# Kernel tuning notes

Hardware: AMD Instinct MI355X
Metric: run time of the kernel (lower is better)

Reference implementation:

```python
import jax, jax.numpy as jnp
import numpy as np

N = 384
C_Z = 128
N_HEADS = 4
HEAD_DIM = C_Z // N_HEADS
LN_EPS = 1e-5


def _layernorm(x, w, b):
    mu = jnp.mean(x, axis=-1, keepdims=True)
    var = jnp.mean(jnp.square(x - mu), axis=-1, keepdims=True)
    return (x - mu) * jax.lax.rsqrt(var + LN_EPS) * w + b


def setup_inputs() -> dict:
    key = jax.random.key(0)
    ks = jax.random.split(key, 6)
    z = jax.random.normal(ks[0], (N, N, C_Z), dtype=jnp.float32)
    # Linear weights stored as [in, out] (transposed vs torch) so y = x @ W + b
    qkv_w = jax.random.normal(ks[1], (C_Z, 3 * C_Z), dtype=jnp.float32) * 0.02
    qkv_b = jnp.zeros((3 * C_Z,), dtype=jnp.float32)
    out_w = jax.random.normal(ks[2], (C_Z, C_Z), dtype=jnp.float32) * 0.02
    out_b = jnp.zeros((C_Z,), dtype=jnp.float32)
    gate_w = jax.random.normal(ks[3], (C_Z, C_Z), dtype=jnp.float32) * 0.02
    gate_b = jnp.zeros((C_Z,), dtype=jnp.float32)
    ln_w = jnp.ones((C_Z,), dtype=jnp.float32)
    ln_b = jnp.zeros((C_Z,), dtype=jnp.float32)
    return {"z": z, "ln_w": ln_w, "ln_b": ln_b, "qkv_w": qkv_w, "qkv_b": qkv_b,
            "out_w": out_w, "out_b": out_b, "gate_w": gate_w, "gate_b": gate_b}


def reference(z, ln_w, ln_b, qkv_w, qkv_b, out_w, out_b, gate_w, gate_b):
    # mode == 'starting': no transpose
    z_norm = _layernorm(z, ln_w, ln_b)                      # [N, N, c_z]
    qkv = (z_norm @ qkv_w + qkv_b).reshape(N, N, 3, N_HEADS, HEAD_DIM)
    q, k, v = qkv[:, :, 0], qkv[:, :, 1], qkv[:, :, 2]      # each [N, N, h, d]
    scale = 1.0 / np.sqrt(HEAD_DIM).astype(np.float32)
    attn = jnp.einsum('inhd,jnhd->nijh', q, k) * scale      # [N, N, N, h]
    attn = jax.nn.softmax(attn, axis=1)                     # softmax over i (dim=1)
    out = jnp.einsum('nijh,jnhd->inhd', attn, v)            # [N, N, h, d]
    out = out.reshape(N, N, C_Z)
    gate = jax.nn.sigmoid(z_norm @ gate_w + gate_b)
    return z + gate * (out @ out_w + out_b)
```

## Files before the change

### kernel.cpp

```cpp
#include <hip/hip_runtime.h>
#include <hip/hip_bf16.h>

#define NN 384
#define CZ 128
#define NH 4
#define HD 32
#define MROWS (NN*NN)

typedef __hip_bfloat16 bf16;
typedef short bf16x8f __attribute__((ext_vector_type(8)));
typedef float f32x4 __attribute__((ext_vector_type(4)));
typedef unsigned short u16x8 __attribute__((ext_vector_type(8)));
typedef unsigned int uint4v __attribute__((ext_vector_type(4)));

__device__ __forceinline__ float b2f(unsigned short u) {
    return __uint_as_float(((unsigned)u) << 16);
}
__device__ __forceinline__ unsigned short f2b(float f) {
    unsigned u = __float_as_uint(f);
    return (unsigned short)((u + 0x7FFFu + ((u >> 16) & 1u)) >> 16);
}
__device__ __forceinline__ unsigned cvt_pk_bf16(float lo, float hi) {
    unsigned r;
    asm("v_cvt_pk_bf16_f32 %0, %1, %2" : "=v"(r) : "v"(lo), "v"(hi));
    return r;
}

__global__ __launch_bounds__(256) void ln_stats_kernel(const float* __restrict__ z,
                                                       float* __restrict__ mu,
                                                       float* __restrict__ rstd) {
    const int wave = threadIdx.x >> 6;
    const int lane = threadIdx.x & 63;
    const int r = blockIdx.x * 4 + wave;
    const float* zr = z + (size_t)r * CZ;
    float x0 = zr[lane], x1 = zr[lane + 64];
    float sum = x0 + x1;
    float sq  = x0 * x0 + x1 * x1;
    #pragma unroll
    for (int o = 32; o > 0; o >>= 1) {
        sum += __shfl_xor(sum, o, 64);
        sq  += __shfl_xor(sq,  o, 64);
    }
    if (lane == 0) {
        const float m   = sum * (1.0f / CZ);
        const float var = sq * (1.0f / CZ) - m * m;
        mu[r]   = m;
        rstd[r] = rsqrtf(var + 1e-5f);
    }
}

__global__ __launch_bounds__(256) void qkv_gemm_mfma_kernel(const float* __restrict__ z,
                                                            const float* __restrict__ mu,
                                                            const float* __restrict__ rstd,
                                                            const float* __restrict__ lnw,
                                                            const float* __restrict__ lnb,
                                                            const float* __restrict__ W,
                                                            const float* __restrict__ bias,
                                                            unsigned short* __restrict__ qkv_t) {
    __shared__ unsigned short Zt[128 * 128];

    const int tid = threadIdx.x;
    const int w = tid >> 6;
    const int l = tid & 63;
    const int col0 = blockIdx.x * 64;
    const int row0 = blockIdx.y * 128;
    const int wcol = w & 1;
    const int wrow = w >> 1;
    const int lm = l & 15;
    const int lq = l >> 4;

    #pragma unroll
    for (int it = 0; it < 8; it++) {
        const int s = it * 256 + tid;
        const int r = s >> 4;
        const int c = (s & 15) ^ (r & 7);
        const int k0 = c * 8;
        const int grow = row0 + r;
        const float m  = mu[grow];
        const float rs = rstd[grow];
        const float4 z0 = *(const float4*)(z + (size_t)grow * CZ + k0);
        const float4 z1 = *(const float4*)(z + (size_t)grow * CZ + k0 + 4);
        const float4 w0 = *(const float4*)(lnw + k0);
        const float4 w1 = *(const float4*)(lnw + k0 + 4);
        const float4 b0 = *(const float4*)(lnb + k0);
        const float4 b1 = *(const float4*)(lnb + k0 + 4);
        u16x8 pk;
        pk[0] = f2b((z0.x - m) * rs * w0.x + b0.x);
        pk[1] = f2b((z0.y - m) * rs * w0.y + b0.y);
        pk[2] = f2b((z0.z - m) * rs * w0.z + b0.z);
        pk[3] = f2b((z0.w - m) * rs * w0.w + b0.w);
        pk[4] = f2b((z1.x - m) * rs * w1.x + b1.x);
        pk[5] = f2b((z1.y - m) * rs * w1.y + b1.y);
        pk[6] = f2b((z1.z - m) * rs * w1.z + b1.z);
        pk[7] = f2b((z1.w - m) * rs * w1.w + b1.w);
        *(u16x8*)&Zt[s * 8] = pk;
    }

    bf16x8f a[2][4];
    #pragma unroll
    for (int fm = 0; fm < 2; fm++) {
        const int gcol = col0 + wcol * 32 + fm * 16 + lm;
        #pragma unroll
        for (int kk = 0; kk < 4; kk++) {
            const int kb = kk * 32 + lq * 8;
            #pragma unroll
            for (int j = 0; j < 8; j++)
                a[fm][kk][j] = (short)f2b(W[(size_t)(kb + j) * (3 * CZ) + gcol]);
        }
    }

    __syncthreads();

    f32x4 acc[2][4];
    #pragma unroll
    for (int fm = 0; fm < 2; fm++)
        #pragma unroll
        for (int fn = 0; fn < 4; fn++)
            acc[fm][fn] = (f32x4){0.0f, 0.0f, 0.0f, 0.0f};

    #pragma unroll
    for (int kk = 0; kk < 4; kk++) {
        bf16x8f bf[4];
        #pragma unroll
        for (int fn = 0; fn < 4; fn++) {
            const int r = wrow * 64 + fn * 16 + lm;
            const int ch = (kk * 4 + lq) ^ (r & 7);
            bf[fn] = *(const bf16x8f*)&Zt[(r * 16 + ch) * 8];
        }
        #pragma unroll
        for (int fm = 0; fm < 2; fm++)
            #pragma unroll
            for (int fn = 0; fn < 4; fn++)
                acc[fm][fn] = __builtin_amdgcn_mfma_f32_16x16x32_bf16(a[fm][kk], bf[fn],
                                                                      acc[fm][fn], 0, 0, 0);
    }

    #pragma unroll
    for (int fm = 0; fm < 2; fm++) {
        const int gc = col0 + wcol * 32 + fm * 16 + lq * 4;
        const float4 b4 = *(const float4*)(bias + gc);
        const int t  = gc >> 7;
        const int hh = (gc & 127) >> 5;
        const int d0 = gc & 31;
        const size_t colbase = (size_t)((t * NH + hh) * NN) * (NN * HD) + d0;
        #pragma unroll
        for (int fn = 0; fn < 4; fn++) {
            const int grow = row0 + wrow * 64 + fn * 16 + lm;
            const int i  = grow / NN;
            const int n0 = grow - i * NN;
            const size_t idx = colbase + (size_t)n0 * (NN * HD) + (size_t)i * HD;
            ushort4 pk;
            pk.x = f2b(acc[fm][fn][0] + b4.x);
            pk.y = f2b(acc[fm][fn][1] + b4.y);
            pk.z = f2b(acc[fm][fn][2] + b4.z);
            pk.w = f2b(acc[fm][fn][3] + b4.w);
            *(ushort4*)(qkv_t + idx) = pk;
        }
    }
}

__global__ __launch_bounds__(256) void attn_mfma_kernel(const unsigned short* __restrict__ qkv_t,
                                                        float* __restrict__ attn_out) {
    __shared__ unsigned short Qf[24 * 512];
    __shared__ unsigned short Kf[24 * 512];
    __shared__ unsigned short Vf[2 * 64 * 8];
    __shared__ float sred[4][32];

    const int b = blockIdx.x;
    const int n = b >> 2;
    const int h = b & 3;
    const int tid = threadIdx.x;
    const int w = tid >> 6;
    const int l = tid & 63;
    const int q = l >> 4;
    const int m = l & 15;
    const size_t base_q = (size_t)((0 * NH + h) * NN + n) * (NN * HD);
    const size_t base_k = (size_t)((1 * NH + h) * NN + n) * (NN * HD);
    const size_t base_v = (size_t)((2 * NH + h) * NN + n) * (NN * HD);
    const float SCALE = 0.17677669529663687f;
    const f32x4 zero = {0.0f, 0.0f, 0.0f, 0.0f};

    #pragma unroll
    for (int it = 0; it < 12; it++) {
        const int s = tid + it * 256;
        const int isK = s >= 1536;
        const int slot = isK ? (s - 1536) : s;
        const int t  = slot >> 6;
        const int l2 = slot & 63;
        const int row = t * 16 + (l2 & 15);
        const int off8 = (l2 >> 4) * 8;
        const u16x8 raw = *(const u16x8*)(qkv_t + (isK ? base_k : base_q) +
                                         (size_t)row * HD + off8);
        unsigned short* dst = (isK ? Kf : Qf) + slot * 8;
        *(u16x8*)dst = raw;
    }
    __syncthreads();

    bf16x8f qreg[6];
    #pragma unroll
    for (int tt = 0; tt < 6; tt++)
        qreg[tt] = *(const bf16x8f*)&Qf[(w + 4 * tt) * 512 + l * 8];

    f32x4 oacc[6][2];
    #pragma unroll
    for (int tt = 0; tt < 6; tt++) {
        oacc[tt][0] = zero;
        oacc[tt][1] = zero;
    }

    const int jj  = tid >> 3;
    const int d0v = (tid & 7) * 4;

    for (int cl = 0; cl < 12; cl++) {
        const bf16x8f ka0 = *(const bf16x8f*)&Kf[(cl * 2 + 0) * 512 + l * 8];
        const bf16x8f ka1 = *(const bf16x8f*)&Kf[(cl * 2 + 1) * 512 + l * 8];

        const ushort4 v4 = *(const ushort4*)(qkv_t + base_v +
                                             (size_t)(cl * 32 + jj) * HD + d0v);

        float sacc[8];
        #pragma unroll
        for (int k = 0; k < 8; k++) sacc[k] = 0.0f;

        unsigned paw[6][4];
        #pragma unroll
        for (int tt = 0; tt < 6; tt++) {
            const f32x4 sT0 = __builtin_amdgcn_mfma_f32_16x16x32_bf16(ka0, qreg[tt], zero, 0, 0, 0);
            const f32x4 sT1 = __builtin_amdgcn_mfma_f32_16x16x32_bf16(ka1, qreg[tt], zero, 0, 0, 0);
            float p[8];
            p[0] = __expf(sT0[0] * SCALE);
            p[1] = __expf(sT0[1] * SCALE);
            p[2] = __expf(sT0[2] * SCALE);
            p[3] = __expf(sT0[3] * SCALE);
            p[4] = __expf(sT1[0] * SCALE);
            p[5] = __expf(sT1[1] * SCALE);
            p[6] = __expf(sT1[2] * SCALE);
            p[7] = __expf(sT1[3] * SCALE);
            #pragma unroll
            for (int k = 0; k < 8; k++) sacc[k] += p[k];
            unsigned c0 = cvt_pk_bf16(p[0], p[1]);
            unsigned c1 = cvt_pk_bf16(p[2], p[3]);
            unsigned c2 = cvt_pk_bf16(p[4], p[5]);
            unsigned c3 = cvt_pk_bf16(p[6], p[7]);
            asm("v_permlane32_swap_b32 %0, %1" : "+v"(c0), "+v"(c2));
            asm("v_permlane32_swap_b32 %0, %1" : "+v"(c1), "+v"(c3));
            asm("v_permlane16_swap_b32 %0, %1" : "+v"(c0), "+v"(c2));
            asm("v_permlane16_swap_b32 %0, %1" : "+v"(c1), "+v"(c3));
            paw[tt][0] = c0; paw[tt][1] = c1; paw[tt][2] = c2; paw[tt][3] = c3;
        }

        #pragma unroll
        for (int k = 0; k < 8; k++) {
            float v = sacc[k];
            v += __shfl_xor(v, 1, 64);
            v += __shfl_xor(v, 2, 64);
            v += __shfl_xor(v, 4, 64);
            v += __shfl_xor(v, 8, 64);
            if (m == 0) sred[w][q * 4 + (k & 3) + (k >> 2) * 16] = v;
        }
        __syncthreads();

        {
            const float inv = 1.0f / (sred[0][jj] + sred[1][jj] + sred[2][jj] + sred[3][jj]);
            const int slotbase = (d0v >> 4) * 64 + (jj >> 3) * 16 + (d0v & 15);
            const int e = jj & 7;
            Vf[(slotbase + 0) * 8 + e] = f2b(b2f(v4.x) * inv);
            Vf[(slotbase + 1) * 8 + e] = f2b(b2f(v4.y) * inv);
            Vf[(slotbase + 2) * 8 + e] = f2b(b2f(v4.z) * inv);
            Vf[(slotbase + 3) * 8 + e] = f2b(b2f(v4.w) * inv);
        }
        __syncthreads();

        const bf16x8f vb0 = *(const bf16x8f*)&Vf[(0 * 64 + l) * 8];
        const bf16x8f vb1 = *(const bf16x8f*)&Vf[(1 * 64 + l) * 8];
        #pragma unroll
        for (int tt = 0; tt < 6; tt++) {
            const uint4v u = {paw[tt][0], paw[tt][1], paw[tt][2], paw[tt][3]};
            const bf16x8f pa = __builtin_bit_cast(bf16x8f, u);
            oacc[tt][0] = __builtin_amdgcn_mfma_f32_16x16x32_bf16(pa, vb0, oacc[tt][0], 0, 0, 0);
            oacc[tt][1] = __builtin_amdgcn_mfma_f32_16x16x32_bf16(pa, vb1, oacc[tt][1], 0, 0, 0);
        }
    }

    #pragma unroll
    for (int tt = 0; tt < 6; tt++) {
        const int it = w + 4 * tt;
        #pragma unroll
        for (int dt = 0; dt < 2; dt++) {
            #pragma unroll
            for (int r = 0; r < 4; r++) {
                const int i = it * 16 + q * 4 + r;
                attn_out[((size_t)i * NN + n) * CZ + h * HD + dt * 16 + m] = oacc[tt][dt][r];
            }
        }
    }
}

__global__ __launch_bounds__(256) void final_mfma_kernel(const float* __restrict__ z,
                                                         const float* __restrict__ mu,
                                                         const float* __restrict__ rstd,
                                                         const float* __restrict__ lnw,
                                                         const float* __restrict__ lnb,
                                                         const float* __restrict__ gate_w,
                                                         const float* __restrict__ gate_b,
                                                         const float* __restrict__ out_w,
                                                         const float* __restrict__ out_b,
                                                         float* out) {
    __shared__ unsigned short Zt[64 * 128];
    __shared__ unsigned short At[64 * 128];

    const int tid = threadIdx.x;
    const int w = tid >> 6;
    const int l = tid & 63;
    const int lm = l & 15;
    const int lq = l >> 4;
    const int row0 = blockIdx.x * 64;

    #pragma unroll
    for (int it = 0; it < 4; it++) {
        const int s = it * 256 + tid;
        const int r = s >> 4;
        const int c = (s & 15) ^ (r & 7);
        const int k0 = c * 8;
        const int grow = row0 + r;
        const float m  = mu[grow];
        const float rs = rstd[grow];
        const size_t gi = (size_t)grow * CZ + k0;
        const float4 z0 = *(const float4*)(z + gi);
        const float4 z1 = *(const float4*)(z + gi + 4);
        const float4 a0 = *(const float4*)(out + gi);
        const float4 a1 = *(const float4*)(out + gi + 4);
        const float4 w0 = *(const float4*)(lnw + k0);
        const float4 w1 = *(const float4*)(lnw + k0 + 4);
        const float4 b0 = *(const float4*)(lnb + k0);
        const float4 b1 = *(const float4*)(lnb + k0 + 4);
        u16x8 pz, pa;
        pz[0] = f2b((z0.x - m) * rs * w0.x + b0.x);
        pz[1] = f2b((z0.y - m) * rs * w0.y + b0.y);
        pz[2] = f2b((z0.z - m) * rs * w0.z + b0.z);
        pz[3] = f2b((z0.w - m) * rs * w0.w + b0.w);
        pz[4] = f2b((z1.x - m) * rs * w1.x + b1.x);
        pz[5] = f2b((z1.y - m) * rs * w1.y + b1.y);
        pz[6] = f2b((z1.z - m) * rs * w1.z + b1.z);
        pz[7] = f2b((z1.w - m) * rs * w1.w + b1.w);
        pa[0] = f2b(a0.x); pa[1] = f2b(a0.y); pa[2] = f2b(a0.z); pa[3] = f2b(a0.w);
        pa[4] = f2b(a1.x); pa[5] = f2b(a1.y); pa[6] = f2b(a1.z); pa[7] = f2b(a1.w);
        *(u16x8*)&Zt[s * 8] = pz;
        *(u16x8*)&At[s * 8] = pa;
    }

    bf16x8f gw[2][4], ow[2][4];
    #pragma unroll
    for (int fm = 0; fm < 2; fm++) {
        const int gcol = w * 32 + fm * 16 + lm;
        #pragma unroll
        for (int kk = 0; kk < 4; kk++) {
            const int kb = kk * 32 + lq * 8;
            #pragma unroll
            for (int j = 0; j < 8; j++) {
                gw[fm][kk][j] = (short)f2b(gate_w[(size_t)(kb + j) * CZ + gcol]);
                ow[fm][kk][j] = (short)f2b(out_w [(size_t)(kb + j) * CZ + gcol]);
            }
        }
    }

    __syncthreads();

    f32x4 acc1[2][4], acc2[2][4];
    #pragma unroll
    for (int fm = 0; fm < 2; fm++)
        #pragma unroll
        for (int fn = 0; fn < 4; fn++) {
            acc1[fm][fn] = (f32x4){0.0f, 0.0f, 0.0f, 0.0f};
            acc2[fm][fn] = (f32x4){0.0f, 0.0f, 0.0f, 0.0f};
        }

    #pragma unroll
    for (int kk = 0; kk < 4; kk++) {
        bf16x8f bz[4], ba[4];
        #pragma unroll
        for (int fn = 0; fn < 4; fn++) {
            const int r = fn * 16 + lm;
            const int ch = (kk * 4 + lq) ^ (r & 7);
            bz[fn] = *(const bf16x8f*)&Zt[(r * 16 + ch) * 8];
            ba[fn] = *(const bf16x8f*)&At[(r * 16 + ch) * 8];
        }
        #pragma unroll
        for (int fm = 0; fm < 2; fm++)
            #pragma unroll
            for (int fn = 0; fn < 4; fn++) {
                acc1[fm][fn] = __builtin_amdgcn_mfma_f32_16x16x32_bf16(gw[fm][kk], bz[fn],
                                                                       acc1[fm][fn], 0, 0, 0);
                acc2[fm][fn] = __builtin_amdgcn_mfma_f32_16x16x32_bf16(ow[fm][kk], ba[fn],
                                                                       acc2[fm][fn], 0, 0, 0);
            }
    }

    #pragma unroll
    for (int fm = 0; fm < 2; fm++) {
        const int gc = w * 32 + fm * 16 + lq * 4;
        const float4 gb4 = *(const float4*)(gate_b + gc);
        const float4 ob4 = *(const float4*)(out_b + gc);
        #pragma unroll
        for (int fn = 0; fn < 4; fn++) {
            const int grow = row0 + fn * 16 + lm;
            const size_t idx = (size_t)grow * CZ + gc;
            const float4 z4 = *(const float4*)(z + idx);
            float4 o;
            o.x = z4.x + (1.0f / (1.0f + __expf(-(acc1[fm][fn][0] + gb4.x)))) * (acc2[fm][fn][0] + ob4.x);
            o.y = z4.y + (1.0f / (1.0f + __expf(-(acc1[fm][fn][1] + gb4.y)))) * (acc2[fm][fn][1] + ob4.y);
            o.z = z4.z + (1.0f / (1.0f + __expf(-(acc1[fm][fn][2] + gb4.z)))) * (acc2[fm][fn][2] + ob4.z);
            o.w = z4.w + (1.0f / (1.0f + __expf(-(acc1[fm][fn][3] + gb4.w)))) * (acc2[fm][fn][3] + ob4.w);
            *(float4*)(out + idx) = o;
        }
    }
}

extern "C" void kernel_launch(void* const* d_in, const int* in_sizes, int n_in,
                              void* d_out, int out_size, void* d_ws, size_t ws_size,
                              hipStream_t stream) {
    const float* z      = (const float*)d_in[0];
    const float* ln_w   = (const float*)d_in[1];
    const float* ln_b   = (const float*)d_in[2];
    const float* qkv_w  = (const float*)d_in[3];
    const float* qkv_b  = (const float*)d_in[4];
    const float* out_w  = (const float*)d_in[5];
    const float* out_b  = (const float*)d_in[6];
    const float* gate_w = (const float*)d_in[7];
    const float* gate_b = (const float*)d_in[8];
    float* out = (float*)d_out;

    float* ws = (float*)d_ws;
    float* mu_buf   = ws;
    float* rstd_buf = ws + MROWS;
    unsigned short* qkv_t = (unsigned short*)(ws + 2 * MROWS);

    ln_stats_kernel<<<MROWS / 4, 256, 0, stream>>>(z, mu_buf, rstd_buf);
    qkv_gemm_mfma_kernel<<<dim3(6, MROWS / 128), 256, 0, stream>>>(z, mu_buf, rstd_buf,
                                                                   ln_w, ln_b, qkv_w, qkv_b, qkv_t);
    attn_mfma_kernel<<<NN * NH, 256, 0, stream>>>(qkv_t, out);
    final_mfma_kernel<<<MROWS / 64, 256, 0, stream>>>(z, mu_buf, rstd_buf, ln_w, ln_b,
                                                      gate_w, gate_b, out_w, out_b, out);
}
```

Baseline: 396.5 us.

## Fuse LayerNorm stats into GEMMs and software-pipeline attention PV step

Drops the separate LayerNorm statistics kernel. Each row's mean and rstd are now recomputed inside the QKV and final GEMM tiles through 16-lane shuffle reductions, which saves a launch and the mu/rstd round trip through global memory. The attention kernel loads Q straight into registers instead of staging it in LDS, and uses a raw exp2 with the scale folded in. It also double-buffers V and the probability fragments so the PV MFMA of one chunk overlaps the score computation of the next, removing one barrier per iteration. The cost is more registers from keeping two sets of P fragments, and redundant LN statistics work in the final kernel.

```diff
diff --git a/kernel.cpp b/kernel.cpp
--- a/kernel.cpp
+++ b/kernel.cpp
@@ -25,33 +25,13 @@
     asm("v_cvt_pk_bf16_f32 %0, %1, %2" : "=v"(r) : "v"(lo), "v"(hi));
     return r;
 }
-
-__global__ __launch_bounds__(256) void ln_stats_kernel(const float* __restrict__ z,
-                                                       float* __restrict__ mu,
-                                                       float* __restrict__ rstd) {
-    const int wave = threadIdx.x >> 6;
-    const int lane = threadIdx.x & 63;
-    const int r = blockIdx.x * 4 + wave;
-    const float* zr = z + (size_t)r * CZ;
-    float x0 = zr[lane], x1 = zr[lane + 64];
-    float sum = x0 + x1;
-    float sq  = x0 * x0 + x1 * x1;
-    #pragma unroll
-    for (int o = 32; o > 0; o >>= 1) {
-        sum += __shfl_xor(sum, o, 64);
-        sq  += __shfl_xor(sq,  o, 64);
-    }
-    if (lane == 0) {
-        const float m   = sum * (1.0f / CZ);
-        const float var = sq * (1.0f / CZ) - m * m;
-        mu[r]   = m;
-        rstd[r] = rsqrtf(var + 1e-5f);
-    }
+__device__ __forceinline__ float fexp2(float x) {
+    float r;
+    asm("v_exp_f32 %0, %1" : "=v"(r) : "v"(x));
+    return r;
 }
 
 __global__ __launch_bounds__(256) void qkv_gemm_mfma_kernel(const float* __restrict__ z,
-                                                            const float* __restrict__ mu,
-                                                            const float* __restrict__ rstd,
                                                             const float* __restrict__ lnw,
                                                             const float* __restrict__ lnb,
                                                             const float* __restrict__ W,
@@ -76,23 +56,31 @@
         const int c = (s & 15) ^ (r & 7);
         const int k0 = c * 8;
         const int grow = row0 + r;
-        const float m  = mu[grow];
-        const float rs = rstd[grow];
         const float4 z0 = *(const float4*)(z + (size_t)grow * CZ + k0);
         const float4 z1 = *(const float4*)(z + (size_t)grow * CZ + k0 + 4);
+        float sum = z0.x + z0.y + z0.z + z0.w + z1.x + z1.y + z1.z + z1.w;
+        float sq  = z0.x*z0.x + z0.y*z0.y + z0.z*z0.z + z0.w*z0.w
+                  + z1.x*z1.x + z1.y*z1.y + z1.z*z1.z + z1.w*z1.w;
+        #pragma unroll
+        for (int o = 1; o < 16; o <<= 1) {
+            sum += __shfl_xor(sum, o, 64);
+            sq  += __shfl_xor(sq,  o, 64);
+        }
+        const float mval = sum * (1.0f / CZ);
+        const float rs   = rsqrtf(sq * (1.0f / CZ) - mval * mval + 1e-5f);
         const float4 w0 = *(const float4*)(lnw + k0);
         const float4 w1 = *(const float4*)(lnw + k0 + 4);
         const float4 b0 = *(const float4*)(lnb + k0);
         const float4 b1 = *(const float4*)(lnb + k0 + 4);
         u16x8 pk;
-        pk[0] = f2b((z0.x - m) * rs * w0.x + b0.x);
-        pk[1] = f2b((z0.y - m) * rs * w0.y + b0.y);
-        pk[2] = f2b((z0.z - m) * rs * w0.z + b0.z);
-        pk[3] = f2b((z0.w - m) * rs * w0.w + b0.w);
-        pk[4] = f2b((z1.x - m) * rs * w1.x + b1.x);
-        pk[5] = f2b((z1.y - m) * rs * w1.y + b1.y);
-        pk[6] = f2b((z1.z - m) * rs * w1.z + b1.z);
-        pk[7] = f2b((z1.w - m) * rs * w1.w + b1.w);
+        pk[0] = f2b((z0.x - mval) * rs * w0.x + b0.x);
+        pk[1] = f2b((z0.y - mval) * rs * w0.y + b0.y);
+        pk[2] = f2b((z0.z - mval) * rs * w0.z + b0.z);
+        pk[3] = f2b((z0.w - mval) * rs * w0.w + b0.w);
+        pk[4] = f2b((z1.x - mval) * rs * w1.x + b1.x);
+        pk[5] = f2b((z1.y - mval) * rs * w1.y + b1.y);
+        pk[6] = f2b((z1.z - mval) * rs * w1.z + b1.z);
+        pk[7] = f2b((z1.w - mval) * rs * w1.w + b1.w);
         *(u16x8*)&Zt[s * 8] = pk;
     }
 
@@ -161,10 +149,9 @@
 
 __global__ __launch_bounds__(256) void attn_mfma_kernel(const unsigned short* __restrict__ qkv_t,
                                                         float* __restrict__ attn_out) {
-    __shared__ unsigned short Qf[24 * 512];
     __shared__ unsigned short Kf[24 * 512];
-    __shared__ unsigned short Vf[2 * 64 * 8];
-    __shared__ float sred[4][32];
+    __shared__ unsigned short Vf[2][1024];
+    __shared__ float sred[2][4][32];
 
     const int b = blockIdx.x;
     const int n = b >> 2;
@@ -177,29 +164,26 @@
     const size_t base_q = (size_t)((0 * NH + h) * NN + n) * (NN * HD);
     const size_t base_k = (size_t)((1 * NH + h) * NN + n) * (NN * HD);
     const size_t base_v = (size_t)((2 * NH + h) * NN + n) * (NN * HD);
-    const float SCALE = 0.17677669529663687f;
+    const float SC2 = 0.17677669529663687f * 1.4426950408889634f;
     const f32x4 zero = {0.0f, 0.0f, 0.0f, 0.0f};
 
     #pragma unroll
-    for (int it = 0; it < 12; it++) {
-        const int s = tid + it * 256;
-        const int isK = s >= 1536;
-        const int slot = isK ? (s - 1536) : s;
+    for (int it = 0; it < 6; it++) {
+        const int slot = tid + it * 256;
         const int t  = slot >> 6;
         const int l2 = slot & 63;
         const int row = t * 16 + (l2 & 15);
         const int off8 = (l2 >> 4) * 8;
-        const u16x8 raw = *(const u16x8*)(qkv_t + (isK ? base_k : base_q) +
-                                         (size_t)row * HD + off8);
-        unsigned short* dst = (isK ? Kf : Qf) + slot * 8;
-        *(u16x8*)dst = raw;
+        *(u16x8*)(Kf + slot * 8) =
+            *(const u16x8*)(qkv_t + base_k + (size_t)row * HD + off8);
+    }
+    bf16x8f qreg[6];
+    #pragma unroll
+    for (int tt = 0; tt < 6; tt++) {
+        const int row = (w + 4 * tt) * 16 + m;
+        qreg[tt] = *(const bf16x8f*)(qkv_t + base_q + (size_t)row * HD + q * 8);
     }
     __syncthreads();
-
-    bf16x8f qreg[6];
-    #pragma unroll
-    for (int tt = 0; tt < 6; tt++)
-        qreg[tt] = *(const bf16x8f*)&Qf[(w + 4 * tt) * 512 + l * 8];
 
     f32x4 oacc[6][2];
     #pragma unroll
@@ -208,13 +192,17 @@
         oacc[tt][1] = zero;
     }
 
+    unsigned pawA[6][4], pawB[6][4];
     const int jj  = tid >> 3;
     const int d0v = (tid & 7) * 4;
-
+    const int slotbase = (d0v >> 4) * 64 + (jj >> 3) * 16 + (d0v & 15);
+    const int e = jj & 7;
+
+    #pragma unroll
     for (int cl = 0; cl < 12; cl++) {
+        const int buf = cl & 1;
         const bf16x8f ka0 = *(const bf16x8f*)&Kf[(cl * 2 + 0) * 512 + l * 8];
         const bf16x8f ka1 = *(const bf16x8f*)&Kf[(cl * 2 + 1) * 512 + l * 8];
-
         const ushort4 v4 = *(const ushort4*)(qkv_t + base_v +
                                              (size_t)(cl * 32 + jj) * HD + d0v);
 
@@ -222,20 +210,19 @@
         #pragma unroll
         for (int k = 0; k < 8; k++) sacc[k] = 0.0f;
 
-        unsigned paw[6][4];
         #pragma unroll
         for (int tt = 0; tt < 6; tt++) {
             const f32x4 sT0 = __builtin_amdgcn_mfma_f32_16x16x32_bf16(ka0, qreg[tt], zero, 0, 0, 0);
             const f32x4 sT1 = __builtin_amdgcn_mfma_f32_16x16x32_bf16(ka1, qreg[tt], zero, 0, 0, 0);
             float p[8];
-            p[0] = __expf(sT0[0] * SCALE);
-            p[1] = __expf(sT0[1] * SCALE);
-            p[2] = __expf(sT0[2] * SCALE);
-            p[3] = __expf(sT0[3] * SCALE);
-            p[4] = __expf(sT1[0] * SCALE);
-            p[5] = __expf(sT1[1] * SCALE);
-            p[6] = __expf(sT1[2] * SCALE);
-            p[7] = __expf(sT1[3] * SCALE);
+            p[0] = fexp2(sT0[0] * SC2);
+            p[1] = fexp2(sT0[1] * SC2);
+            p[2] = fexp2(sT0[2] * SC2);
+            p[3] = fexp2(sT0[3] * SC2);
+            p[4] = fexp2(sT1[0] * SC2);
+            p[5] = fexp2(sT1[1] * SC2);
+            p[6] = fexp2(sT1[2] * SC2);
+            p[7] = fexp2(sT1[3] * SC2);
             #pragma unroll
             for (int k = 0; k < 8; k++) sacc[k] += p[k];
             unsigned c0 = cvt_pk_bf16(p[0], p[1]);
@@ -246,7 +233,11 @@
             asm("v_permlane32_swap_b32 %0, %1" : "+v"(c1), "+v"(c3));
             asm("v_permlane16_swap_b32 %0, %1" : "+v"(c0), "+v"(c2));
             asm("v_permlane16_swap_b32 %0, %1" : "+v"(c1), "+v"(c3));
-            paw[tt][0] = c0; paw[tt][1] = c1; paw[tt][2] = c2; paw[tt][3] = c3;
+            if (buf == 0) {
+                pawA[tt][0] = c0; pawA[tt][1] = c1; pawA[tt][2] = c2; pawA[tt][3] = c3;
+            } else {
+                pawB[tt][0] = c0; pawB[tt][1] = c1; pawB[tt][2] = c2; pawB[tt][3] = c3;
+            }
         }
 
         #pragma unroll
@@ -256,26 +247,41 @@
             v += __shfl_xor(v, 2, 64);
             v += __shfl_xor(v, 4, 64);
             v += __shfl_xor(v, 8, 64);
-            if (m == 0) sred[w][q * 4 + (k & 3) + (k >> 2) * 16] = v;
+            if (m == 0) sred[buf][w][q * 4 + (k & 3) + (k >> 2) * 16] = v;
         }
         __syncthreads();
 
         {
-            const float inv = 1.0f / (sred[0][jj] + sred[1][jj] + sred[2][jj] + sred[3][jj]);
-            const int slotbase = (d0v >> 4) * 64 + (jj >> 3) * 16 + (d0v & 15);
-            const int e = jj & 7;
-            Vf[(slotbase + 0) * 8 + e] = f2b(b2f(v4.x) * inv);
-            Vf[(slotbase + 1) * 8 + e] = f2b(b2f(v4.y) * inv);
-            Vf[(slotbase + 2) * 8 + e] = f2b(b2f(v4.z) * inv);
-            Vf[(slotbase + 3) * 8 + e] = f2b(b2f(v4.w) * inv);
-        }
-        __syncthreads();
-
-        const bf16x8f vb0 = *(const bf16x8f*)&Vf[(0 * 64 + l) * 8];
-        const bf16x8f vb1 = *(const bf16x8f*)&Vf[(1 * 64 + l) * 8];
+            const float inv = 1.0f / (sred[buf][0][jj] + sred[buf][1][jj] +
+                                      sred[buf][2][jj] + sred[buf][3][jj]);
+            Vf[buf][(slotbase + 0) * 8 + e] = f2b(b2f(v4.x) * inv);
+            Vf[buf][(slotbase + 1) * 8 + e] = f2b(b2f(v4.y) * inv);
+            Vf[buf][(slotbase + 2) * 8 + e] = f2b(b2f(v4.z) * inv);
+            Vf[buf][(slotbase + 3) * 8 + e] = f2b(b2f(v4.w) * inv);
+        }
+
+        if (cl > 0) {
+            const bf16x8f vb0 = *(const bf16x8f*)&Vf[buf ^ 1][(0 * 64 + l) * 8];
+            const bf16x8f vb1 = *(const bf16x8f*)&Vf[buf ^ 1][(1 * 64 + l) * 8];
+            #pragma unroll
+            for (int tt = 0; tt < 6; tt++) {
+                uint4v u;
+                if (buf == 1) { u = (uint4v){pawA[tt][0], pawA[tt][1], pawA[tt][2], pawA[tt][3]}; }
+                else          { u = (uint4v){pawB[tt][0], pawB[tt][1], pawB[tt][2], pawB[tt][3]}; }
+                const bf16x8f pa = __builtin_bit_cast(bf16x8f, u);
+                oacc[tt][0] = __builtin_amdgcn_mfma_f32_16x16x32_bf16(pa, vb0, oacc[tt][0], 0, 0, 0);
+                oacc[tt][1] = __builtin_amdgcn_mfma_f32_16x16x32_bf16(pa, vb1, oacc[tt][1], 0, 0, 0);
+            }
+        }
+    }
+
+    __syncthreads();
+    {
+        const bf16x8f vb0 = *(const bf16x8f*)&Vf[1][(0 * 64 + l) * 8];
+        const bf16x8f vb1 = *(const bf16x8f*)&Vf[1][(1 * 64 + l) * 8];
         #pragma unroll
         for (int tt = 0; tt < 6; tt++) {
-            const uint4v u = {paw[tt][0], paw[tt][1], paw[tt][2], paw[tt][3]};
+            const uint4v u = {pawB[tt][0], pawB[tt][1], pawB[tt][2], pawB[tt][3]};
             const bf16x8f pa = __builtin_bit_cast(bf16x8f, u);
             oacc[tt][0] = __builtin_amdgcn_mfma_f32_16x16x32_bf16(pa, vb0, oacc[tt][0], 0, 0, 0);
             oacc[tt][1] = __builtin_amdgcn_mfma_f32_16x16x32_bf16(pa, vb1, oacc[tt][1], 0, 0, 0);
@@ -297,8 +303,6 @@
 }
 
 __global__ __launch_bounds__(256) void final_mfma_kernel(const float* __restrict__ z,
-                                                         const float* __restrict__ mu,
-                                                         const float* __restrict__ rstd,
                                                          const float* __restrict__ lnw,
                                                          const float* __restrict__ lnb,
                                                          const float* __restrict__ gate_w,
@@ -323,26 +327,34 @@
         const int c = (s & 15) ^ (r & 7);
         const int k0 = c * 8;
         const int grow = row0 + r;
-        const float m  = mu[grow];
-        const float rs = rstd[grow];
         const size_t gi = (size_t)grow * CZ + k0;
         const float4 z0 = *(const float4*)(z + gi);
         const float4 z1 = *(const float4*)(z + gi + 4);
         const float4 a0 = *(const float4*)(out + gi);
         const float4 a1 = *(const float4*)(out + gi + 4);
+        float sum = z0.x + z0.y + z0.z + z0.w + z1.x + z1.y + z1.z + z1.w;
+        float sq  = z0.x*z0.x + z0.y*z0.y + z0.z*z0.z + z0.w*z0.w
+                  + z1.x*z1.x + z1.y*z1.y + z1.z*z1.z + z1.w*z1.w;
+        #pragma unroll
+        for (int o = 1; o < 16; o <<= 1) {
+            sum += __shfl_xor(sum, o, 64);
+            sq  += __shfl_xor(sq,  o, 64);
+        }
+        const float mval = sum * (1.0f / CZ);
+        const float rs   = rsqrtf(sq * (1.0f / CZ) - mval * mval + 1e-5f);
         const float4 w0 = *(const float4*)(lnw + k0);
         const float4 w1 = *(const float4*)(lnw + k0 + 4);
         const float4 b0 = *(const float4*)(lnb + k0);
         const float4 b1 = *(const float4*)(lnb + k0 + 4);
         u16x8 pz, pa;
-        pz[0] = f2b((z0.x - m) * rs * w0.x + b0.x);
-        pz[1] = f2b((z0.y - m) * rs * w0.y + b0.y);
-        pz[2] = f2b((z0.z - m) * rs * w0.z + b0.z);
-        pz[3] = f2b((z0.w - m) * rs * w0.w + b0.w);
-        pz[4] = f2b((z1.x - m) * rs * w1.x + b1.x);
-        pz[5] = f2b((z1.y - m) * rs * w1.y + b1.y);
-        pz[6] = f2b((z1.z - m) * rs * w1.z + b1.z);
-        pz[7] = f2b((z1.w - m) * rs * w1.w + b1.w);
+        pz[0] = f2b((z0.x - mval) * rs * w0.x + b0.x);
+        pz[1] = f2b((z0.y - mval) * rs * w0.y + b0.y);
+        pz[2] = f2b((z0.z - mval) * rs * w0.z + b0.z);
+        pz[3] = f2b((z0.w - mval) * rs * w0.w + b0.w);
+        pz[4] = f2b((z1.x - mval) * rs * w1.x + b1.x);
+        pz[5] = f2b((z1.y - mval) * rs * w1.y + b1.y);
+        pz[6] = f2b((z1.z - mval) * rs * w1.z + b1.z);
+        pz[7] = f2b((z1.w - mval) * rs * w1.w + b1.w);
         pa[0] = f2b(a0.x); pa[1] = f2b(a0.y); pa[2] = f2b(a0.z); pa[3] = f2b(a0.w);
         pa[4] = f2b(a1.x); pa[5] = f2b(a1.y); pa[6] = f2b(a1.z); pa[7] = f2b(a1.w);
         *(u16x8*)&Zt[s * 8] = pz;
@@ -430,15 +442,11 @@
     const float* gate_b = (const float*)d_in[8];
     float* out = (float*)d_out;
 
-    float* ws = (float*)d_ws;
-    float* mu_buf   = ws;
-    float* rstd_buf = ws + MROWS;
-    unsigned short* qkv_t = (unsigned short*)(ws + 2 * MROWS);
-
-    ln_stats_kernel<<<MROWS / 4, 256, 0, stream>>>(z, mu_buf, rstd_buf);
-    qkv_gemm_mfma_kernel<<<dim3(6, MROWS / 128), 256, 0, stream>>>(z, mu_buf, rstd_buf,
-                                                                   ln_w, ln_b, qkv_w, qkv_b, qkv_t);
+    unsigned short* qkv_t = (unsigned short*)d_ws;
+
+    qkv_gemm_mfma_kernel<<<dim3(6, MROWS / 128), 256, 0, stream>>>(z, ln_w, ln_b,
+                                                                   qkv_w, qkv_b, qkv_t);
     attn_mfma_kernel<<<NN * NH, 256, 0, stream>>>(qkv_t, out);
-    final_mfma_kernel<<<MROWS / 64, 256, 0, stream>>>(z, mu_buf, rstd_buf, ln_w, ln_b,
+    final_mfma_kernel<<<MROWS / 64, 256, 0, stream>>>(z, ln_w, ln_b,
                                                       gate_w, gate_b, out_w, out_b, out);
 }
```

Result: slower. 412.0 us (+3.9%).
